# Performance work log

Hardware: AMD Instinct MI355X
Metric: run time of the kernel (lower is better)

## Reference

```python
import jax, jax.numpy as jnp
import numpy as np

C, NH, NW = 32, 64, 256  # channels, canvas height, canvas width (from __init__)
B, N = 64, 900_000       # batch size, number of voxels


def setup_inputs() -> dict:
    key = jax.random.key(0)
    kf, kp = jax.random.split(key)
    features = jax.random.normal(kf, (C, N), dtype=jnp.float32)
    # unique (b, h, w) cells -> no duplicate scatter indices (matches torch determinism)
    flat = jax.random.permutation(kp, B * NH * NW)[:N].astype(jnp.int32)
    b = flat // (NH * NW)
    rem = flat % (NH * NW)
    h = rem // NW
    w = rem % NW
    coords = jnp.stack([b, h, w], axis=1)  # [N, 3] int32
    return {"features": features, "coords": coords, "batch_size": B}


def reference(features, coords, batch_size):
    # features: [C, N]; coords: [N, 3] = (batch, h, w)
    # Single fused scatter over all batches: flatten (b, h, w) -> one index.
    flat_idx = coords[:, 0] * (NH * NW) + coords[:, 1] * NW + coords[:, 2]  # [N]
    canvas = jnp.zeros((batch_size * NH * NW, C), dtype=features.dtype)
    canvas = canvas.at[flat_idx].set(features.T)  # scatter voxel features
    # -> [B, C, NH, NW]
    return canvas.reshape(batch_size, NH, NW, C).transpose(0, 3, 1, 2)
```

## Files before the change

### kernel.cpp

```cpp
#include <hip/hip_runtime.h>

#define CC 32
#define BB 64
#define NHH 64
#define NWW 256
#define PLANE (NHH * NWW)
#define BSTRIDE (CC * PLANE)
#define NCELLS (BB * PLANE)

__global__ void pss_scatter_direct(const float* __restrict__ features,
                                   const int* __restrict__ coords,
                                   float* __restrict__ out, int N) {
    int n = blockIdx.x * blockDim.x + threadIdx.x;
    if (n >= N) return;
    int b = coords[3 * n + 0];
    int h = coords[3 * n + 1];
    int w = coords[3 * n + 2];
    int base = b * BSTRIDE + h * NWW + w;
#pragma unroll
    for (int c = 0; c < CC; ++c)
        out[base + c * PLANE] = features[c * N + n];
}

__global__ __launch_bounds__(256) void pss_zero(int4* __restrict__ p, int n4) {
    int i = blockIdx.x * blockDim.x + threadIdx.x;
    if (i < n4) p[i] = make_int4(0, 0, 0, 0);
}

__global__ void pss_invmap(const int* __restrict__ coords,
                           int* __restrict__ invmap, int N) {
    int n = blockIdx.x * blockDim.x + threadIdx.x;
    if (n >= N) return;
    int b = coords[3 * n + 0];
    int h = coords[3 * n + 1];
    int w = coords[3 * n + 2];
    invmap[b * PLANE + h * NWW + w] = n + 1;
}

__global__ __launch_bounds__(256) void pss_transpose_wp(
        const float* __restrict__ features, float* __restrict__ featT, int N) {
    __shared__ float lds[4 * CC * 66];

    int lane = threadIdx.x & 63;
    int wid = threadIdx.x >> 6;
    int n0 = blockIdx.x * 256 + wid * 64;
    if (n0 >= N) return;

    float* wl = &lds[wid * CC * 66];

    int n = n0 + lane;
    bool okn = (n < N);

    float f[CC];
#pragma unroll
    for (int c = 0; c < CC; ++c)
        f[c] = okn ? __builtin_nontemporal_load(&features[(size_t)c * N + n])
                   : 0.0f;

#pragma unroll
    for (int c = 0; c < CC; ++c)
        wl[c * 66 + lane] = f[c];

    float4* dstv = (float4*)featT;
    int cq = lane & 7;
    int nlb = lane >> 3;
#pragma unroll
    for (int j = 0; j < 8; ++j) {
        int nl = nlb + 8 * j;
        if (n0 + nl < N) {
            float4 v;
            v.x = wl[(4 * cq + 0) * 66 + nl];
            v.y = wl[(4 * cq + 1) * 66 + nl];
            v.z = wl[(4 * cq + 2) * 66 + nl];
            v.w = wl[(4 * cq + 3) * 66 + nl];
            dstv[(size_t)n0 * 8 + lane + 64 * j] = v;
        }
    }
}

__global__ __launch_bounds__(256) void pss_gather_emit(
        const float* __restrict__ featT, const int* __restrict__ invmap,
        float* __restrict__ out) {
    __shared__ float lds[NWW * (CC + 1)];

    int row = blockIdx.x;
    int b = row / NHH;
    int h = row % NHH;
    int t = threadIdx.x;

    int inv = invmap[(size_t)row * NWW + t];

    if (inv > 0) {
        const float4* src = (const float4*)(featT + (size_t)(inv - 1) * CC);
#pragma unroll
        for (int k = 0; k < CC / 4; ++k) {
            float4 v = src[k];
            lds[t * (CC + 1) + 4 * k + 0] = v.x;
            lds[t * (CC + 1) + 4 * k + 1] = v.y;
            lds[t * (CC + 1) + 4 * k + 2] = v.z;
            lds[t * (CC + 1) + 4 * k + 3] = v.w;
        }
    } else {
#pragma unroll
        for (int k = 0; k < CC; ++k)
            lds[t * (CC + 1) + k] = 0.0f;
    }

    __syncthreads();

    size_t obase = (size_t)b * BSTRIDE + (size_t)h * NWW + t;
#pragma unroll
    for (int c = 0; c < CC; ++c) {
        float v = lds[t * (CC + 1) + c];
        __builtin_nontemporal_store(v, &out[obase + (size_t)c * PLANE]);
    }
}

extern "C" void kernel_launch(void* const* d_in, const int* in_sizes, int n_in,
                              void* d_out, int out_size, void* d_ws, size_t ws_size,
                              hipStream_t stream) {
    const float* features = (const float*)d_in[0];
    const int* coords = (const int*)d_in[1];
    float* out = (float*)d_out;
    const int N = in_sizes[1] / 3;

    const size_t invmap_bytes = (size_t)NCELLS * sizeof(int);
    const size_t featT_bytes = (size_t)N * CC * sizeof(float);

    if (ws_size < invmap_bytes + featT_bytes) {
        hipMemsetAsync(d_out, 0, (size_t)out_size * sizeof(float), stream);
        int blocks = (N + 255) / 256;
        pss_scatter_direct<<<blocks, 256, 0, stream>>>(features, coords, out, N);
        return;
    }

    int* invmap = (int*)d_ws;
    float* featT = (float*)((char*)d_ws + invmap_bytes);

    pss_zero<<<(NCELLS / 4 + 255) / 256, 256, 0, stream>>>((int4*)invmap,
                                                           NCELLS / 4);

    pss_invmap<<<(N + 255) / 256, 256, 0, stream>>>(coords, invmap, N);

    pss_transpose_wp<<<(N + 255) / 256, 256, 0, stream>>>(features, featT, N);

    pss_gather_emit<<<BB * NHH, 256, 0, stream>>>(featT, invmap, out);
}
```

Before: 97.79 us.

## Make transpose kernel persistent with software-pipelined register prefetch

The feature transpose kernel becomes a grid-stride persistent kernel with a fixed grid of 1024 blocks. Each wave loads the next tile's features into registers while it writes the current tile out from LDS, so global loads overlap with stores. This replaces one short-lived wave per tile. The cost is a fixed grid that may underfill or unbalance the GPU, and the kernel has no barrier between the LDS writes and reads across loop iterations.

Measured after the change: 99.52 us. No clear change (+1.8%).

```diff
diff --git a/kernel.cpp b/kernel.cpp
--- a/kernel.cpp
+++ b/kernel.cpp
@@ -7,6 +7,7 @@
 #define PLANE (NHH * NWW)
 #define BSTRIDE (CC * PLANE)
 #define NCELLS (BB * PLANE)
+#define TGRID 1024
 
 __global__ void pss_scatter_direct(const float* __restrict__ features,
                                    const int* __restrict__ coords,
@@ -37,44 +38,66 @@
     invmap[b * PLANE + h * NWW + w] = n + 1;
 }
 
-__global__ __launch_bounds__(256) void pss_transpose_wp(
-        const float* __restrict__ features, float* __restrict__ featT, int N) {
+__global__ __launch_bounds__(256) void pss_transpose_pp(
+        const float* __restrict__ features, float* __restrict__ featT,
+        int N, int ntiles) {
     __shared__ float lds[4 * CC * 66];
 
     int lane = threadIdx.x & 63;
     int wid = threadIdx.x >> 6;
-    int n0 = blockIdx.x * 256 + wid * 64;
-    if (n0 >= N) return;
-
     float* wl = &lds[wid * CC * 66];
 
-    int n = n0 + lane;
-    bool okn = (n < N);
+    const int nwaves = TGRID * 4;
+    int T = blockIdx.x * 4 + wid;
+    if (T >= ntiles) return;
 
     float f[CC];
+
+    {
+        int n = T * 64 + lane;
+        bool ok = (n < N);
 #pragma unroll
-    for (int c = 0; c < CC; ++c)
-        f[c] = okn ? __builtin_nontemporal_load(&features[(size_t)c * N + n])
-                   : 0.0f;
-
-#pragma unroll
-    for (int c = 0; c < CC; ++c)
-        wl[c * 66 + lane] = f[c];
+        for (int c = 0; c < CC; ++c)
+            f[c] = ok ? __builtin_nontemporal_load(&features[(size_t)c * N + n])
+                      : 0.0f;
+    }
 
     float4* dstv = (float4*)featT;
     int cq = lane & 7;
     int nlb = lane >> 3;
+
+    while (true) {
 #pragma unroll
-    for (int j = 0; j < 8; ++j) {
-        int nl = nlb + 8 * j;
-        if (n0 + nl < N) {
-            float4 v;
-            v.x = wl[(4 * cq + 0) * 66 + nl];
-            v.y = wl[(4 * cq + 1) * 66 + nl];
-            v.z = wl[(4 * cq + 2) * 66 + nl];
-            v.w = wl[(4 * cq + 3) * 66 + nl];
-            dstv[(size_t)n0 * 8 + lane + 64 * j] = v;
+        for (int c = 0; c < CC; ++c)
+            wl[c * 66 + lane] = f[c];
+
+        int Tn = T + nwaves;
+        if (Tn < ntiles) {
+            int n = Tn * 64 + lane;
+            bool ok = (n < N);
+#pragma unroll
+            for (int c = 0; c < CC; ++c)
+                f[c] = ok ? __builtin_nontemporal_load(
+                                &features[(size_t)c * N + n])
+                          : 0.0f;
         }
+
+        int n0 = T * 64;
+#pragma unroll
+        for (int j = 0; j < 8; ++j) {
+            int nl = nlb + 8 * j;
+            if (n0 + nl < N) {
+                float4 v;
+                v.x = wl[(4 * cq + 0) * 66 + nl];
+                v.y = wl[(4 * cq + 1) * 66 + nl];
+                v.z = wl[(4 * cq + 2) * 66 + nl];
+                v.w = wl[(4 * cq + 3) * 66 + nl];
+                dstv[(size_t)n0 * 8 + lane + 64 * j] = v;
+            }
+        }
+
+        if (Tn >= ntiles) break;
+        T = Tn;
     }
 }
 
@@ -128,7 +151,7 @@
     const size_t featT_bytes = (size_t)N * CC * sizeof(float);
 
     if (ws_size < invmap_bytes + featT_bytes) {
-        hipMemsetAsync(d_out, 0, (size_t)out_size * sizeof(float), stream);
+        (void)hipMemsetAsync(d_out, 0, (size_t)out_size * sizeof(float), stream);
         int blocks = (N + 255) / 256;
         pss_scatter_direct<<<blocks, 256, 0, stream>>>(features, coords, out, N);
         return;
@@ -142,7 +165,8 @@
 
     pss_invmap<<<(N + 255) / 256, 256, 0, stream>>>(coords, invmap, N);
 
-    pss_transpose_wp<<<(N + 255) / 256, 256, 0, stream>>>(features, featT, N);
+    int ntiles = (N + 63) / 64;
+    pss_transpose_pp<<<TGRID, 256, 0, stream>>>(features, featT, N, ntiles);
 
     pss_gather_emit<<<BB * NHH, 256, 0, stream>>>(featT, invmap, out);
 }
```
